# Optimization experiments

Hardware: AMD Instinct MI355X
Metric: run time of the kernel (lower is better)

The kernel has to match this reference:

```python
import jax, jax.numpy as jnp
import numpy as np

NEG_SLOPE = 0.01  # nn.LeakyReLU default

N = 100000
E = 1600000
D_IN = 128
D_OUT = 128


def setup_inputs() -> dict:
    key = jax.random.key(0)
    ks = jax.random.split(key, 8)
    features = jax.random.normal(ks[0], (N, D_IN), dtype=jnp.float32)
    adj_rows = jax.random.randint(ks[1], (E,), 0, N, dtype=jnp.int64)
    adj_cols = jax.random.randint(ks[2], (E,), 0, N, dtype=jnp.int64)
    adj_vals = jax.random.uniform(ks[3], (E,), dtype=jnp.float32)
    s1 = 1.0 / np.sqrt(D_IN)
    W1 = jax.random.uniform(ks[4], (D_IN, D_OUT), jnp.float32, -s1, s1)
    b1 = jax.random.uniform(ks[5], (D_OUT,), jnp.float32, -s1, s1)
    W2 = jax.random.uniform(ks[6], (D_IN, D_OUT), jnp.float32, -s1, s1)
    b2 = jax.random.uniform(ks[7], (D_OUT,), jnp.float32, -s1, s1)
    return {"features": features, "adj_rows": adj_rows, "adj_cols": adj_cols,
            "adj_vals": adj_vals, "W1": W1, "b1": b1, "W2": W2, "b2": b2}


def reference(features, adj_rows, adj_cols, adj_vals, W1, b1, W2, b2):
    # h_neigh = adj @ features  (COO SpMM via gather + segment_sum)
    msgs = adj_vals[:, None] * features[adj_cols]          # [E, D_IN]
    h_neigh = jax.ops.segment_sum(msgs, adj_rows, num_segments=features.shape[0])
    term1 = (features + h_neigh) @ W1 + b1                 # W1(features + h_neigh)
    term2 = (features * h_neigh) @ W2 + b2                 # W2(features * h_neigh)
    pre = term1 + term2
    return jnp.where(pre >= 0, pre, NEG_SLOPE * pre)       # leaky_relu
```

## Files before the change

kernel.cpp:

```cpp
#include <hip/hip_runtime.h>

#define D 128
#define BM 64

typedef short short8 __attribute__((ext_vector_type(8)));
typedef unsigned short ushort8_t __attribute__((ext_vector_type(8)));
typedef float f32x4 __attribute__((ext_vector_type(4)));

__device__ __forceinline__ unsigned short f2bf(float x) {
    unsigned u = __float_as_uint(x);
    unsigned r = (u + 0x7fffu + ((u >> 16) & 1u)) >> 16;
    return (unsigned short)r;
}
__device__ __forceinline__ float bf2f(unsigned short u) {
    return __uint_as_float(((unsigned)u) << 16);
}

__global__ __launch_bounds__(256) void fconv_kernel(
    const float4* __restrict__ feat4, ushort4* __restrict__ fbf4, int total)
{
    int i = blockIdx.x * 256 + threadIdx.x;
    if (i < total) {
        float4 v = feat4[i];
        fbf4[i] = make_ushort4(f2bf(v.x), f2bf(v.y), f2bf(v.z), f2bf(v.w));
    }
}

__global__ __launch_bounds__(256) void wconv_kernel(
    const float* __restrict__ W1, const float* __restrict__ W2,
    unsigned short* __restrict__ WT)
{
    int idx = blockIdx.x * 256 + threadIdx.x;
    int c = idx & 127;
    int k = idx >> 7;
    float w = (k < 128) ? W1[k * 128 + c] : W2[(k - 128) * 128 + c];
    WT[c * 256 + k] = f2bf(w);
}


__global__ __launch_bounds__(256) void bucket_hist_kernel(
    const int* __restrict__ rows, int* __restrict__ bcnt, int E, int nb, int epb)
{
    __shared__ int cnt[1024];
    int t = threadIdx.x;
    for (int i = t; i < nb; i += 256) cnt[i] = 0;
    __syncthreads();
    int e0 = blockIdx.x * epb;
    int e1 = e0 + epb; if (e1 > E) e1 = E;
    for (int e = e0 + t; e < e1; e += 256) atomicAdd(&cnt[rows[e] >> 7], 1);
    __syncthreads();
    for (int i = t; i < nb; i += 256)
        if (cnt[i]) atomicAdd(&bcnt[i], cnt[i]);
}

__global__ __launch_bounds__(1024) void bucket_scan_kernel(
    const int* __restrict__ bcnt, int* __restrict__ bstart,
    int* __restrict__ bcur, int nb, int E)
{
    __shared__ int wsum[16];
    int tid = threadIdx.x, lane = tid & 63, wid = tid >> 6;
    int x = (tid < nb) ? bcnt[tid] : 0;
    int v = x;
    #pragma unroll
    for (int off = 1; off < 64; off <<= 1) {
        int y = __shfl_up(v, off, 64);
        if (lane >= off) v += y;
    }
    if (lane == 63) wsum[wid] = v;
    __syncthreads();
    if (wid == 0 && lane < 16) {
        int s = wsum[lane];
        #pragma unroll
        for (int off = 1; off < 16; off <<= 1) {
            int y = __shfl_up(s, off, 64);
            if (lane >= off) s += y;
        }
        wsum[lane] = s;
    }
    __syncthreads();
    int wexcl = wid ? wsum[wid - 1] : 0;
    int excl = wexcl + v - x;
    if (tid < nb) { bstart[tid] = excl; bcur[tid] = excl; }
    if (tid == 0) bstart[nb] = E;
}

__global__ __launch_bounds__(256) void bucket_scatter_kernel(
    const int* __restrict__ rows, const int* __restrict__ cols,
    const float* __restrict__ vals, int* __restrict__ bcur,
    uint2* __restrict__ bsedge, int E, int nb)
{
    __shared__ int cnt[1024];
    __shared__ int base[1024];
    int t = threadIdx.x;
    int e0 = blockIdx.x * 4096;
    for (int i = t; i < nb; i += 256) cnt[i] = 0;
    __syncthreads();
    #pragma unroll
    for (int q = 0; q < 16; ++q) {
        int e = e0 + t + q * 256;
        if (e < E) atomicAdd(&cnt[rows[e] >> 7], 1);
    }
    __syncthreads();
    for (int i = t; i < nb; i += 256) {
        int c = cnt[i];
        if (c) { base[i] = atomicAdd(&bcur[i], c); cnt[i] = 0; }
    }
    __syncthreads();
    #pragma unroll
    for (int q = 0; q < 16; ++q) {
        int e = e0 + t + q * 256;
        if (e < E) {
            int r = rows[e];
            int b = r >> 7;
            int pos = base[b] + atomicAdd(&cnt[b], 1);
            bsedge[pos] = make_uint2(((unsigned)(r & 127) << 17) | (unsigned)cols[e],
                                     __float_as_uint(vals[e]));
        }
    }
}

__global__ __launch_bounds__(256) void bucket_sort_kernel(
    const uint2* __restrict__ bsedge,
    const int* __restrict__ bstart,
    uint2* __restrict__ sedge,
    int* __restrict__ row_start,
    int N, int E)
{
    __shared__ int cnt[128];
    __shared__ int base[128];
    const int b = blockIdx.x;
    const int t = threadIdx.x;
    const int s = bstart[b], e = bstart[b + 1];
    if (t < 128) cnt[t] = 0;
    __syncthreads();
    for (int j = s + t; j < e; j += 256)
        atomicAdd(&cnt[bsedge[j].x >> 17], 1);
    __syncthreads();
    if (t < 64) {
        int c0 = cnt[2 * t], c1 = cnt[2 * t + 1];
        int pair = c0 + c1;
        int v = pair;
        #pragma unroll
        for (int off = 1; off < 64; off <<= 1) {
            int y = __shfl_up(v, off, 64);
            if (t >= off) v += y;
        }
        int excl = v - pair;
        base[2 * t]     = excl;
        base[2 * t + 1] = excl + c0;
        cnt[2 * t] = 0;
        cnt[2 * t + 1] = 0;
    }
    __syncthreads();
    const int r0 = b << 7;
    if (t < 128 && r0 + t < N) row_start[r0 + t] = s + base[t];
    if (b == 0 && t == 0) row_start[N] = E;
    for (int j = s + t; j < e; j += 256) {
        uint2 ed = bsedge[j];
        int rl = ed.x >> 17;
        int p = atomicAdd(&cnt[rl], 1);
        sedge[s + base[rl] + p] = make_uint2(ed.x & 0x1FFFFu, ed.y);
    }
}

__global__ __launch_bounds__(256) void spmm_gemm16_kernel(
    const float4* __restrict__ feat4,
    const ushort8_t* __restrict__ fbf8,
    const int* __restrict__ row_start,
    const uint2* __restrict__ sedge,
    const unsigned short* __restrict__ WT,
    const float* __restrict__ b1, const float* __restrict__ b2,
    float* __restrict__ out, int N)
{
    __shared__ __align__(16) unsigned char am_raw[16 * 512];

    const int tid = threadIdx.x;
    const int block0 = blockIdx.x * 16;
    const int rq = tid >> 4;
    const int l  = tid & 15;

    int row = block0 + rq;
    float acc[8] = {};
    float f[8] = {};
    if (row < N) {
        int s = row_start[row];
        int e = row_start[row + 1];
        int j = s;
        for (; j + 3 < e; j += 4) {
            uint2 e0 = sedge[j],     e1 = sedge[j + 1];
            uint2 e2 = sedge[j + 2], e3 = sedge[j + 3];
            ushort8_t f0 = fbf8[(size_t)e0.x * 16 + l];
            ushort8_t f1 = fbf8[(size_t)e1.x * 16 + l];
            ushort8_t f2 = fbf8[(size_t)e2.x * 16 + l];
            ushort8_t f3 = fbf8[(size_t)e3.x * 16 + l];
            float v0 = __uint_as_float(e0.y), v1 = __uint_as_float(e1.y);
            float v2 = __uint_as_float(e2.y), v3 = __uint_as_float(e3.y);
            #pragma unroll
            for (int q = 0; q < 8; ++q) {
                acc[q] = fmaf(v0, bf2f(f0[q]), acc[q]);
                acc[q] = fmaf(v1, bf2f(f1[q]), acc[q]);
                acc[q] = fmaf(v2, bf2f(f2[q]), acc[q]);
                acc[q] = fmaf(v3, bf2f(f3[q]), acc[q]);
            }
        }
        for (; j < e; ++j) {
            uint2 e0 = sedge[j];
            float v = __uint_as_float(e0.y);
            ushort8_t f0 = fbf8[(size_t)e0.x * 16 + l];
            #pragma unroll
            for (int q = 0; q < 8; ++q) acc[q] = fmaf(v, bf2f(f0[q]), acc[q]);
        }
        float4 fa = feat4[(size_t)row * 32 + 2 * l];
        float4 fb = feat4[(size_t)row * 32 + 2 * l + 1];
        f[0] = fa.x; f[1] = fa.y; f[2] = fa.z; f[3] = fa.w;
        f[4] = fb.x; f[5] = fb.y; f[6] = fb.z; f[7] = fb.w;
    }
    ushort8_t av, mv;
    #pragma unroll
    for (int q = 0; q < 8; ++q) {
        av[q] = f2bf(f[q] + acc[q]);
        mv[q] = f2bf(f[q] * acc[q]);
    }
    {
        int swz = (rq & 7) << 4;
        unsigned char* rowp = am_raw + rq * 512;
        *(ushort8_t*)(rowp + ((16 * l) ^ swz))       = av;
        *(ushort8_t*)(rowp + 256 + ((16 * l) ^ swz)) = mv;
    }
    __syncthreads();

    const int lane = tid & 63;
    const int w    = tid >> 6;
    const int l15  = lane & 15;
    const int lk   = lane >> 4;
    const int rswz = (l15 & 7) << 4;

    f32x4 gacc[2] = {};
    const char* WTc = (const char*)WT;
    const unsigned char* arow = am_raw + l15 * 512;

    #pragma unroll
    for (int ks = 0; ks < 8; ++ks) {
        int kbyte = ks * 64 + lk * 16;
        short8 a = *(const short8*)(arow + (kbyte ^ rswz));
        #pragma unroll
        for (int nc = 0; nc < 2; ++nc) {
            int col = w * 32 + nc * 16 + l15;
            short8 b = *(const short8*)(WTc + col * 512 + kbyte);
            gacc[nc] = __builtin_amdgcn_mfma_f32_16x16x32_bf16(a, b, gacc[nc], 0, 0, 0);
        }
    }

    #pragma unroll
    for (int nc = 0; nc < 2; ++nc) {
        int col = w * 32 + nc * 16 + l15;
        float bias = b1[col] + b2[col];
        int rbase = block0 + lk * 4;
        #pragma unroll
        for (int r = 0; r < 4; ++r) {
            int orow = rbase + r;
            if (orow < N) {
                float v = gacc[nc][r] + bias;
                out[orow * 128 + col] = (v >= 0.f) ? v : 0.01f * v;
            }
        }
    }
}

__global__ __launch_bounds__(256) void spmm_ab_kernel(
    const float4* __restrict__ feat4,
    const ushort8_t* __restrict__ fbf8,
    const int* __restrict__ row_start,
    const uint2* __restrict__ sedge,
    unsigned char* __restrict__ ambf, int N)
{
    int t = blockIdx.x * 256 + threadIdx.x;
    int row = t >> 4;
    int l   = t & 15;
    if (row >= N) return;

    int s = row_start[row];
    int e = row_start[row + 1];

    float acc[8] = {};
    int j = s;
    for (; j + 1 < e; j += 2) {
        uint2 e0 = sedge[j], e1 = sedge[j + 1];
        float v0 = __uint_as_float(e0.y), v1 = __uint_as_float(e1.y);
        ushort8_t f0 = fbf8[(size_t)e0.x * 16 + l];
        ushort8_t f1 = fbf8[(size_t)e1.x * 16 + l];
        #pragma unroll
        for (int q = 0; q < 8; ++q) {
            acc[q] = fmaf(v0, bf2f(f0[q]), acc[q]);
            acc[q] = fmaf(v1, bf2f(f1[q]), acc[q]);
        }
    }
    if (j < e) {
        uint2 e0 = sedge[j];
        float v = __uint_as_float(e0.y);
        ushort8_t f = fbf8[(size_t)e0.x * 16 + l];
        #pragma unroll
        for (int q = 0; q < 8; ++q) acc[q] = fmaf(v, bf2f(f[q]), acc[q]);
    }

    float4 fa = feat4[(size_t)row * 32 + 2 * l];
    float4 fb = feat4[(size_t)row * 32 + 2 * l + 1];
    float f[8] = { fa.x, fa.y, fa.z, fa.w, fb.x, fb.y, fb.z, fb.w };

    ushort8_t av, mv;
    #pragma unroll
    for (int q = 0; q < 8; ++q) {
        av[q] = f2bf(f[q] + acc[q]);
        mv[q] = f2bf(f[q] * acc[q]);
    }

    int swz = (row & 7) << 4;
    unsigned char* rowp = ambf + (size_t)row * 512;
    *(ushort8_t*)(rowp + ((16 * l) ^ swz))       = av;
    *(ushort8_t*)(rowp + 256 + ((16 * l) ^ swz)) = mv;
}

__global__ __launch_bounds__(256) void mfma_gemm2_kernel(
    const unsigned char* __restrict__ ambf,
    const unsigned short* __restrict__ WT,
    const float* __restrict__ b1, const float* __restrict__ b2,
    float* __restrict__ out, int N)
{
    __shared__ __align__(16) unsigned char am_raw[64 * 512];

    const int tid = threadIdx.x;
    const int block0 = blockIdx.x * BM;

    const short8* src = (const short8*)(ambf + (size_t)block0 * 512);
    short8* dst = (short8*)am_raw;
    #pragma unroll
    for (int it = 0; it < 8; ++it) {
        int idx = tid + it * 256;
        dst[idx] = src[idx];
    }
    __syncthreads();

    const int lane = tid & 63;
    const int w    = tid >> 6;
    const int wr   = w >> 1;
    const int wc   = w & 1;
    const int l15  = lane & 15;
    const int lk   = lane >> 4;
    const int rswz = (l15 & 7) << 4;

    f32x4 acc[2][4] = {};

    const char* WTc = (const char*)WT;
    const unsigned char* arow0 = am_raw + (wr * 32 + l15) * 512;
    const unsigned char* arow1 = arow0 + 16 * 512;

    #pragma unroll
    for (int ks = 0; ks < 8; ++ks) {
        int kbyte = ks * 64 + lk * 16;
        int akoff = kbyte ^ rswz;
        short8 a0 = *(const short8*)(arow0 + akoff);
        short8 a1 = *(const short8*)(arow1 + akoff);
        short8 bfr[4];
        #pragma unroll
        for (int nc = 0; nc < 4; ++nc) {
            int col = wc * 64 + nc * 16 + l15;
            bfr[nc] = *(const short8*)(WTc + col * 512 + kbyte);
        }
        #pragma unroll
        for (int nc = 0; nc < 4; ++nc) {
            acc[0][nc] = __builtin_amdgcn_mfma_f32_16x16x32_bf16(a0, bfr[nc], acc[0][nc], 0, 0, 0);
            acc[1][nc] = __builtin_amdgcn_mfma_f32_16x16x32_bf16(a1, bfr[nc], acc[1][nc], 0, 0, 0);
        }
    }

    #pragma unroll
    for (int nc = 0; nc < 4; ++nc) {
        int col = wc * 64 + nc * 16 + l15;
        float bias = b1[col] + b2[col];
        #pragma unroll
        for (int mr = 0; mr < 2; ++mr) {
            int rbase = block0 + wr * 32 + mr * 16 + lk * 4;
            #pragma unroll
            for (int r = 0; r < 4; ++r) {
                int row = rbase + r;
                if (row < N) {
                    float v = acc[mr][nc][r] + bias;
                    out[row * 128 + col] = (v >= 0.f) ? v : 0.01f * v;
                }
            }
        }
    }
}

__global__ __launch_bounds__(256) void hist_kernel(
    const int* __restrict__ rows, int* __restrict__ counts, int E)
{
    int e = blockIdx.x * 256 + threadIdx.x;
    if (e < E) atomicAdd(&counts[rows[e]], 1);
}

__global__ __launch_bounds__(256) void scan_pass1(
    const int* __restrict__ counts, int* __restrict__ btot, int N)
{
    int tid = threadIdx.x;
    int i = blockIdx.x * 1024 + tid * 4;
    int s = 0;
    if (i + 3 < N) {
        int4 v = *(const int4*)(counts + i);
        s = v.x + v.y + v.z + v.w;
    } else {
        for (int q = 0; q < 4; ++q) if (i + q < N) s += counts[i + q];
    }
    #pragma unroll
    for (int off = 32; off >= 1; off >>= 1) s += __shfl_down(s, off, 64);
    __shared__ int ws[4];
    if ((tid & 63) == 0) ws[tid >> 6] = s;
    __syncthreads();
    if (tid == 0) btot[blockIdx.x] = ws[0] + ws[1] + ws[2] + ws[3];
}

__global__ __launch_bounds__(1024) void scan_pass2(
    const int* __restrict__ btot, int* __restrict__ boff, int nb)
{
    __shared__ int wsum[16];
    int tid = threadIdx.x, lane = tid & 63, wid = tid >> 6;
    int x = (tid < nb) ? btot[tid] : 0;
    int v = x;
    #pragma unroll
    for (int off = 1; off < 64; off <<= 1) {
        int y = __shfl_up(v, off, 64);
        if (lane >= off) v += y;
    }
    if (lane == 63) wsum[wid] = v;
    __syncthreads();
    if (wid == 0 && lane < 16) {
        int s = wsum[lane];
        #pragma unroll
        for (int off = 1; off < 16; off <<= 1) {
            int y = __shfl_up(s, off, 64);
            if (lane >= off) s += y;
        }
        wsum[lane] = s;
    }
    __syncthreads();
    int wexcl = wid ? wsum[wid - 1] : 0;
    if (tid < nb) boff[tid] = wexcl + v - x;
}

__global__ __launch_bounds__(256) void scan_pass3(
    int* __restrict__ row_start, int* __restrict__ cursor,
    const int* __restrict__ boff, int N, int E)
{
    int tid = threadIdx.x;
    int base = blockIdx.x * 1024 + tid * 4;
    int c0 = 0, c1 = 0, c2 = 0, c3 = 0;
    if (base + 3 < N) {
        int4 v = *(const int4*)(row_start + base);
        c0 = v.x; c1 = v.y; c2 = v.z; c3 = v.w;
    } else {
        if (base + 0 < N) c0 = row_start[base + 0];
        if (base + 1 < N) c1 = row_start[base + 1];
        if (base + 2 < N) c2 = row_start[base + 2];
        if (base + 3 < N) c3 = row_start[base + 3];
    }
    int s0 = c0, s1 = s0 + c1, s2 = s1 + c2, s3 = s2 + c3;
    int lane = tid & 63, wid = tid >> 6;
    int v = s3;
    #pragma unroll
    for (int off = 1; off < 64; off <<= 1) {
        int y = __shfl_up(v, off, 64);
        if (lane >= off) v += y;
    }
    __shared__ int ws[4];
    if (lane == 63) ws[wid] = v;
    __syncthreads();
    int wexcl = 0;
    for (int q = 0; q < wid; ++q) wexcl += ws[q];
    int texcl = wexcl + (v - s3) + boff[blockIdx.x];
    int e0 = texcl, e1 = texcl + s0, e2 = texcl + s1, e3 = texcl + s2;
    if (base + 0 < N) { row_start[base + 0] = e0; cursor[base + 0] = e0; }
    if (base + 1 < N) { row_start[base + 1] = e1; cursor[base + 1] = e1; }
    if (base + 2 < N) { row_start[base + 2] = e2; cursor[base + 2] = e2; }
    if (base + 3 < N) { row_start[base + 3] = e3; cursor[base + 3] = e3; }
    if (blockIdx.x == 0 && tid == 0) row_start[N] = E;
}

__global__ __launch_bounds__(256) void scatter_sort_kernel(
    const int* __restrict__ rows, const int* __restrict__ cols,
    const float* __restrict__ vals, int* __restrict__ cursor,
    uint2* __restrict__ sedge, int E)
{
    int e = blockIdx.x * 256 + threadIdx.x;
    if (e < E) {
        int r = rows[e];
        int p = atomicAdd(&cursor[r], 1);
        sedge[p] = make_uint2((unsigned)cols[e], __float_as_uint(vals[e]));
    }
}

__global__ __launch_bounds__(256) void spmm_kernel(
    const float2* __restrict__ feat2,
    const int* __restrict__ row_start,
    const uint2* __restrict__ sedge,
    float2* __restrict__ h2, int N)
{
    int gw = (blockIdx.x * 256 + threadIdx.x) >> 6;
    int lane = threadIdx.x & 63;
    if (gw >= N) return;
    int s = row_start[gw];
    int e = row_start[gw + 1];
    float2 acc = make_float2(0.f, 0.f);
    int j = s;
    for (; j + 1 < e; j += 2) {
        uint2 e0 = sedge[j], e1 = sedge[j + 1];
        float v0 = __uint_as_float(e0.y), v1 = __uint_as_float(e1.y);
        float2 f0 = feat2[(size_t)e0.x * 64 + lane];
        float2 f1 = feat2[(size_t)e1.x * 64 + lane];
        acc.x = fmaf(v0, f0.x, acc.x);
        acc.y = fmaf(v0, f0.y, acc.y);
        acc.x = fmaf(v1, f1.x, acc.x);
        acc.y = fmaf(v1, f1.y, acc.y);
    }
    if (j < e) {
        uint2 e0 = sedge[j];
        float v = __uint_as_float(e0.y);
        float2 f = feat2[(size_t)e0.x * 64 + lane];
        acc.x = fmaf(v, f.x, acc.x);
        acc.y = fmaf(v, f.y, acc.y);
    }
    h2[(size_t)gw * 64 + lane] = acc;
}

__global__ __launch_bounds__(256) void mfma_gemm_kernel(
    const float4* __restrict__ feat4, const float4* __restrict__ h4,
    const unsigned short* __restrict__ WT,
    const float* __restrict__ b1, const float* __restrict__ b2,
    float* __restrict__ out, int N)
{
    __shared__ __align__(16) unsigned char am_raw[64 * 512];
    const int tid = threadIdx.x;
    const int block0 = blockIdx.x * BM;
    #pragma unroll
    for (int it = 0; it < 8; ++it) {
        int idx  = tid + it * 256;
        int node = idx >> 5;
        int p    = idx & 31;
        int g    = block0 + node;
        float4 fv = make_float4(0.f, 0.f, 0.f, 0.f);
        float4 hv = make_float4(0.f, 0.f, 0.f, 0.f);
        if (g < N) { fv = feat4[g * 32 + p]; hv = h4[g * 32 + p]; }
        ushort4 av = make_ushort4(f2bf(fv.x + hv.x), f2bf(fv.y + hv.y),
                                  f2bf(fv.z + hv.z), f2bf(fv.w + hv.w));
        ushort4 mv = make_ushort4(f2bf(fv.x * hv.x), f2bf(fv.y * hv.y),
                                  f2bf(fv.z * hv.z), f2bf(fv.w * hv.w));
        int swz = (node & 7) << 4;
        *(ushort4*)(am_raw + node * 512 + ((p * 8) ^ swz))       = av;
        *(ushort4*)(am_raw + node * 512 + ((256 + p * 8) ^ swz)) = mv;
    }
    __syncthreads();
    const int lane = tid & 63;
    const int w    = tid >> 6;
    const int wr   = w >> 1;
    const int wc   = w & 1;
    const int l15  = lane & 15;
    const int lk   = lane >> 4;
    const int rswz = (l15 & 7) << 4;
    f32x4 acc[2][4] = {};
    const char* WTc = (const char*)WT;
    const unsigned char* arow0 = am_raw + (wr * 32 + l15) * 512;
    const unsigned char* arow1 = arow0 + 16 * 512;
    #pragma unroll
    for (int ks = 0; ks < 8; ++ks) {
        int kbyte = ks * 64 + lk * 16;
        int akoff = kbyte ^ rswz;
        short8 a0 = *(const short8*)(arow0 + akoff);
        short8 a1 = *(const short8*)(arow1 + akoff);
        short8 bfr[4];
        #pragma unroll
        for (int nc = 0; nc < 4; ++nc) {
            int col = wc * 64 + nc * 16 + l15;
            bfr[nc] = *(const short8*)(WTc + col * 512 + kbyte);
        }
        #pragma unroll
        for (int nc = 0; nc < 4; ++nc) {
            acc[0][nc] = __builtin_amdgcn_mfma_f32_16x16x32_bf16(a0, bfr[nc], acc[0][nc], 0, 0, 0);
            acc[1][nc] = __builtin_amdgcn_mfma_f32_16x16x32_bf16(a1, bfr[nc], acc[1][nc], 0, 0, 0);
        }
    }
    #pragma unroll
    for (int nc = 0; nc < 4; ++nc) {
        int col = wc * 64 + nc * 16 + l15;
        float bias = b1[col] + b2[col];
        #pragma unroll
        for (int mr = 0; mr < 2; ++mr) {
            int rbase = block0 + wr * 32 + mr * 16 + lk * 4;
            #pragma unroll
            for (int r = 0; r < 4; ++r) {
                int row = rbase + r;
                if (row < N) {
                    float v = acc[mr][nc][r] + bias;
                    out[row * 128 + col] = (v >= 0.f) ? v : 0.01f * v;
                }
            }
        }
    }
}

__global__ __launch_bounds__(256) void edge_scatter_kernel(
    const float4* __restrict__ feat4, const int* __restrict__ rows,
    const int* __restrict__ cols, const float* __restrict__ vals,
    float* __restrict__ h, int E)
{
    int idx = blockIdx.x * 256 + threadIdx.x;
    if (idx >= E * 32) return;
    int e = idx >> 5;
    int p = idx & 31;
    int r = rows[e];
    int c = cols[e];
    float v = vals[e];
    float4 f = feat4[c * 32 + p];
    float* hr = h + (long long)r * D + p * 4;
    unsafeAtomicAdd(hr + 0, v * f.x);
    unsafeAtomicAdd(hr + 1, v * f.y);
    unsafeAtomicAdd(hr + 2, v * f.z);
    unsafeAtomicAdd(hr + 3, v * f.w);
}

__global__ __launch_bounds__(256) void fused_gemm_kernel(
    const float* __restrict__ feat, const float* __restrict__ h,
    const float* __restrict__ W1, const float* __restrict__ b1,
    const float* __restrict__ W2, const float* __restrict__ b2,
    float* __restrict__ out, int N)
{
    __shared__ float a_lds[BM][D];
    __shared__ float m_lds[BM][D];
    const int tid = threadIdx.x;
    const int block0 = blockIdx.x * BM;
    const float4* feat4 = (const float4*)feat;
    const float4* h4    = (const float4*)h;
    #pragma unroll
    for (int it = 0; it < 8; ++it) {
        int idx  = tid + it * 256;
        int node = idx >> 5;
        int p    = idx & 31;
        int gnode = block0 + node;
        float4 fv = make_float4(0.f, 0.f, 0.f, 0.f);
        float4 hv = make_float4(0.f, 0.f, 0.f, 0.f);
        if (gnode < N) { fv = feat4[gnode * 32 + p]; hv = h4[gnode * 32 + p]; }
        float4 av = make_float4(fv.x + hv.x, fv.y + hv.y, fv.z + hv.z, fv.w + hv.w);
        float4 mv = make_float4(fv.x * hv.x, fv.y * hv.y, fv.z * hv.z, fv.w * hv.w);
        *(float4*)&a_lds[node][p * 4] = av;
        *(float4*)&m_lds[node][p * 4] = mv;
    }
    __syncthreads();
    const int c = tid & 31;
    const int g = tid >> 5;
    float acc[8][4] = {};
    const float4* W1v = (const float4*)W1;
    const float4* W2v = (const float4*)W2;
    for (int k = 0; k < D; ++k) {
        float4 w1 = W1v[k * 32 + c];
        float4 w2 = W2v[k * 32 + c];
        #pragma unroll
        for (int t = 0; t < 8; ++t) {
            float av = a_lds[g + 8 * t][k];
            float mv = m_lds[g + 8 * t][k];
            acc[t][0] = fmaf(av, w1.x, fmaf(mv, w2.x, acc[t][0]));
            acc[t][1] = fmaf(av, w1.y, fmaf(mv, w2.y, acc[t][1]));
            acc[t][2] = fmaf(av, w1.z, fmaf(mv, w2.z, acc[t][2]));
            acc[t][3] = fmaf(av, w1.w, fmaf(mv, w2.w, acc[t][3]));
        }
    }
    float4 bb1 = ((const float4*)b1)[c];
    float4 bb2 = ((const float4*)b2)[c];
    const float bx = bb1.x + bb2.x, by = bb1.y + bb2.y;
    const float bz = bb1.z + bb2.z, bw = bb1.w + bb2.w;
    #pragma unroll
    for (int t = 0; t < 8; ++t) {
        int gnode = block0 + g + 8 * t;
        if (gnode >= N) continue;
        float4 o;
        o.x = acc[t][0] + bx; o.y = acc[t][1] + by;
        o.z = acc[t][2] + bz; o.w = acc[t][3] + bw;
        o.x = (o.x >= 0.f) ? o.x : 0.01f * o.x;
        o.y = (o.y >= 0.f) ? o.y : 0.01f * o.y;
        o.z = (o.z >= 0.f) ? o.z : 0.01f * o.z;
        o.w = (o.w >= 0.f) ? o.w : 0.01f * o.w;
        ((float4*)out)[gnode * 32 + c] = o;
    }
}

extern "C" void kernel_launch(void* const* d_in, const int* in_sizes, int n_in,
                              void* d_out, int out_size, void* d_ws, size_t ws_size,
                              hipStream_t stream) {
    const float* feat = (const float*)d_in[0];
    const int*   rows = (const int*)d_in[1];
    const int*   cols = (const int*)d_in[2];
    const float* vals = (const float*)d_in[3];
    const float* W1   = (const float*)d_in[4];
    const float* b1   = (const float*)d_in[5];
    const float* W2   = (const float*)d_in[6];
    const float* b2   = (const float*)d_in[7];

    const int N = in_sizes[0] / D;
    const int E = in_sizes[1];
    float* out = (float*)d_out;

    const int NBK  = (N + 127) >> 7;
    const int Npad = NBK << 7;

    size_t off = 0;
    unsigned short* featbf = (unsigned short*)d_ws;                off += (size_t)N * D * 2;
    off = (off + 15) & ~(size_t)15;
    uint2* sedge = (uint2*)((char*)d_ws + off);                    off += (size_t)E * 8;
    unsigned short* WT = (unsigned short*)((char*)d_ws + off);     off += 128 * 256 * 2;
    int* row_start = (int*)((char*)d_ws + off);                    off += (size_t)(N + 1) * 4;
    off = (off + 15) & ~(size_t)15;
    uint2* bsedge = (uint2*)((char*)d_ws + off);                   off += (size_t)E * 8;
    int* bcnt   = (int*)((char*)d_ws + off);                       off += (size_t)NBK * 4;
    int* bstart = (int*)((char*)d_ws + off);                       off += (size_t)(NBK + 1) * 4;
    int* bcur   = (int*)((char*)d_ws + off);                       off += (size_t)NBK * 4;
    size_t need1a = off;

    if (ws_size >= need1a && NBK <= 1024 && N <= (1 << 17)) {
        hipMemsetAsync(bcnt, 0, (size_t)NBK * sizeof(int), stream);
        fconv_kernel<<<(N * 32 + 255) / 256, 256, 0, stream>>>(
            (const float4*)feat, (ushort4*)featbf, N * 32);
        wconv_kernel<<<128, 256, 0, stream>>>(W1, W2, WT);
        int epb = (E + 255) / 256;
        bucket_hist_kernel<<<256, 256, 0, stream>>>(rows, bcnt, E, NBK, epb);
        bucket_scan_kernel<<<1, 1024, 0, stream>>>(bcnt, bstart, bcur, NBK, E);
        bucket_scatter_kernel<<<(E + 4095) / 4096, 256, 0, stream>>>(
            rows, cols, vals, bcur, bsedge, E, NBK);
        bucket_sort_kernel<<<NBK, 256, 0, stream>>>(
            bsedge, bstart, sedge, row_start, N, E);
        spmm_gemm16_kernel<<<(N + 15) / 16, 256, 0, stream>>>(
            (const float4*)feat, (const ushort8_t*)featbf, row_start, sedge,
            WT, b1, b2, out, N);
        return;
    }

    const int NB = (N + 1023) / 1024;
    off = 0;
    unsigned char* ambf = (unsigned char*)d_ws;                    off += (size_t)Npad * 512;
    featbf = (unsigned short*)((char*)d_ws + off);                 off += (size_t)N * D * 2;
    off = (off + 15) & ~(size_t)15;
    sedge = (uint2*)((char*)d_ws + off);                           off += (size_t)E * 8;
    WT = (unsigned short*)((char*)d_ws + off);                     off += 128 * 256 * 2;
    row_start = (int*)((char*)d_ws + off);                         off += (size_t)(N + 1) * 4;
    off = (off + 15) & ~(size_t)15;
    int* cursor = (int*)((char*)d_ws + off);                       off += (size_t)N * 4;
    int* btot = (int*)((char*)d_ws + off);                         off += (size_t)NB * 4;
    int* boff = (int*)((char*)d_ws + off);                         off += (size_t)NB * 4;
    size_t need1b = off;

    if (ws_size >= need1b && NB <= 1024) {
        hipMemsetAsync(row_start, 0, (size_t)(N + 1) * sizeof(int), stream);
        fconv_kernel<<<(N * 32 + 255) / 256, 256, 0, stream>>>(
            (const float4*)feat, (ushort4*)featbf, N * 32);
        wconv_kernel<<<128, 256, 0, stream>>>(W1, W2, WT);
        hist_kernel<<<(E + 255) / 256, 256, 0, stream>>>(rows, row_start, E);
        scan_pass1<<<NB, 256, 0, stream>>>(row_start, btot, N);
        scan_pass2<<<1, 1024, 0, stream>>>(btot, boff, NB);
        scan_pass3<<<NB, 256, 0, stream>>>(row_start, cursor, boff, N, E);
        scatter_sort_kernel<<<(E + 255) / 256, 256, 0, stream>>>(
            rows, cols, vals, cursor, sedge, E);
        spmm_ab_kernel<<<(N * 16 + 255) / 256, 256, 0, stream>>>(
            (const float4*)feat, (const ushort8_t*)featbf, row_start, sedge,
            ambf, N);
        mfma_gemm2_kernel<<<(N + BM - 1) / BM, 256, 0, stream>>>(
            ambf, WT, b1, b2, out, N);
        return;
    }

    off = 0;
    float* h = (float*)d_ws;                           off += (size_t)N * D * 4;
    int* row_start2 = (int*)((char*)d_ws + off);       off += (size_t)(N + 1) * 4;
    int* cursor2    = (int*)((char*)d_ws + off);       off += (size_t)N * 4;
    off = (off + 15) & ~(size_t)15;
    uint2* sedge2   = (uint2*)((char*)d_ws + off);     off += (size_t)E * 8;
    off = (off + 15) & ~(size_t)15;
    unsigned short* WT2 = (unsigned short*)((char*)d_ws + off); off += 128 * 256 * 2;
    int* btot2 = (int*)((char*)d_ws + off);            off += (size_t)NB * 4;
    int* boff2 = (int*)((char*)d_ws + off);            off += (size_t)NB * 4;
    size_t need2 = off;

    if (ws_size >= need2 && NB <= 1024) {
        hipMemsetAsync(row_start2, 0, (size_t)(N + 1) * sizeof(int), stream);
        wconv_kernel<<<128, 256, 0, stream>>>(W1, W2, WT2);
        hist_kernel<<<(E + 255) / 256, 256, 0, stream>>>(rows, row_start2, E);
        scan_pass1<<<NB, 256, 0, stream>>>(row_start2, btot2, N);
        scan_pass2<<<1, 1024, 0, stream>>>(btot2, boff2, NB);
        scan_pass3<<<NB, 256, 0, stream>>>(row_start2, cursor2, boff2, N, E);
        scatter_sort_kernel<<<(E + 255) / 256, 256, 0, stream>>>(
            rows, cols, vals, cursor2, sedge2, E);
        spmm_kernel<<<(N * 64 + 255) / 256, 256, 0, stream>>>(
            (const float2*)feat, row_start2, sedge2, (float2*)h, N);
        mfma_gemm_kernel<<<(N + BM - 1) / BM, 256, 0, stream>>>(
            (const float4*)feat, (const float4*)h, WT2, b1, b2, out, N);
        return;
    }

    size_t hbytes = (size_t)N * D * sizeof(float);
    float* hh = (ws_size >= hbytes) ? (float*)d_ws : out;
    hipMemsetAsync(hh, 0, hbytes, stream);
    edge_scatter_kernel<<<((size_t)E * 32 + 255) / 256, 256, 0, stream>>>(
        (const float4*)feat, rows, cols, vals, hh, E);
    fused_gemm_kernel<<<(N + BM - 1) / BM, 256, 0, stream>>>(
        feat, hh, W1, b1, W2, b2, out, N);
}
```

Baseline: 184.6 us.

## Fuse preprocessing kernels, unroll gather by 8, read own features in bf16

Merges the feature bf16 conversion, weight transpose/convert, and row-bucket histogram into one prep kernel, saving two launches and letting the independent work overlap. The SpMM gather loop gains an 8-wide unrolled path that issues more independent loads before accumulating, to hide gather latency. The row's own features are now read from the bf16 copy instead of fp32, which halves that read but adds rounding error to the features+h and features*h terms.

```diff
diff --git a/kernel.cpp b/kernel.cpp
--- a/kernel.cpp
+++ b/kernel.cpp
@@ -14,6 +14,41 @@
 }
 __device__ __forceinline__ float bf2f(unsigned short u) {
     return __uint_as_float(((unsigned)u) << 16);
+}
+
+__global__ __launch_bounds__(256) void prep_kernel(
+    const float4* __restrict__ feat4, ushort4* __restrict__ fbf4, int nf4,
+    const float* __restrict__ W1, const float* __restrict__ W2,
+    unsigned short* __restrict__ WT,
+    const int* __restrict__ rows, int* __restrict__ bcnt,
+    int E, int nb, int epb)
+{
+    __shared__ int cnt[1024];
+    const int t = threadIdx.x;
+    const int b = blockIdx.x;
+    for (int i = t; i < nb; i += 256) cnt[i] = 0;
+    __syncthreads();
+
+    int e0 = b * epb;
+    int e1 = e0 + epb; if (e1 > E) e1 = E;
+    for (int e = e0 + t; e < e1; e += 256) atomicAdd(&cnt[rows[e] >> 7], 1);
+
+    for (int i = b * 256 + t; i < nf4; i += 256 * 256) {
+        float4 v = feat4[i];
+        fbf4[i] = make_ushort4(f2bf(v.x), f2bf(v.y), f2bf(v.z), f2bf(v.w));
+    }
+
+    if (b < 128) {
+        int idx = b * 256 + t;
+        int c = idx & 127;
+        int k = idx >> 7;
+        float w = (k < 128) ? W1[k * 128 + c] : W2[(k - 128) * 128 + c];
+        WT[c * 256 + k] = f2bf(w);
+    }
+
+    __syncthreads();
+    for (int i = t; i < nb; i += 256)
+        if (cnt[i]) atomicAdd(&bcnt[i], cnt[i]);
 }
 
 __global__ __launch_bounds__(256) void fconv_kernel(
@@ -35,22 +70,6 @@
     int k = idx >> 7;
     float w = (k < 128) ? W1[k * 128 + c] : W2[(k - 128) * 128 + c];
     WT[c * 256 + k] = f2bf(w);
-}
-
-
-__global__ __launch_bounds__(256) void bucket_hist_kernel(
-    const int* __restrict__ rows, int* __restrict__ bcnt, int E, int nb, int epb)
-{
-    __shared__ int cnt[1024];
-    int t = threadIdx.x;
-    for (int i = t; i < nb; i += 256) cnt[i] = 0;
-    __syncthreads();
-    int e0 = blockIdx.x * epb;
-    int e1 = e0 + epb; if (e1 > E) e1 = E;
-    for (int e = e0 + t; e < e1; e += 256) atomicAdd(&cnt[rows[e] >> 7], 1);
-    __syncthreads();
-    for (int i = t; i < nb; i += 256)
-        if (cnt[i]) atomicAdd(&bcnt[i], cnt[i]);
 }
 
 __global__ __launch_bounds__(1024) void bucket_scan_kernel(
@@ -164,7 +183,6 @@
 }
 
 __global__ __launch_bounds__(256) void spmm_gemm16_kernel(
-    const float4* __restrict__ feat4,
     const ushort8_t* __restrict__ fbf8,
     const int* __restrict__ row_start,
     const uint2* __restrict__ sedge,
@@ -186,6 +204,22 @@
         int s = row_start[row];
         int e = row_start[row + 1];
         int j = s;
+        for (; j + 7 < e; j += 8) {
+            uint2 ed[8];
+            #pragma unroll
+            for (int q = 0; q < 8; ++q) ed[q] = sedge[j + q];
+            ushort8_t ff[8];
+            #pragma unroll
+            for (int q = 0; q < 8; ++q)
+                ff[q] = fbf8[(size_t)ed[q].x * 16 + l];
+            #pragma unroll
+            for (int q = 0; q < 8; ++q) {
+                float v = __uint_as_float(ed[q].y);
+                #pragma unroll
+                for (int p = 0; p < 8; ++p)
+                    acc[p] = fmaf(v, bf2f(ff[q][p]), acc[p]);
+            }
+        }
         for (; j + 3 < e; j += 4) {
             uint2 e0 = sedge[j],     e1 = sedge[j + 1];
             uint2 e2 = sedge[j + 2], e3 = sedge[j + 3];
@@ -196,11 +230,11 @@
             float v0 = __uint_as_float(e0.y), v1 = __uint_as_float(e1.y);
             float v2 = __uint_as_float(e2.y), v3 = __uint_as_float(e3.y);
             #pragma unroll
-            for (int q = 0; q < 8; ++q) {
-                acc[q] = fmaf(v0, bf2f(f0[q]), acc[q]);
-                acc[q] = fmaf(v1, bf2f(f1[q]), acc[q]);
-                acc[q] = fmaf(v2, bf2f(f2[q]), acc[q]);
-                acc[q] = fmaf(v3, bf2f(f3[q]), acc[q]);
+            for (int p = 0; p < 8; ++p) {
+                acc[p] = fmaf(v0, bf2f(f0[p]), acc[p]);
+                acc[p] = fmaf(v1, bf2f(f1[p]), acc[p]);
+                acc[p] = fmaf(v2, bf2f(f2[p]), acc[p]);
+                acc[p] = fmaf(v3, bf2f(f3[p]), acc[p]);
             }
         }
         for (; j < e; ++j) {
@@ -208,12 +242,11 @@
             float v = __uint_as_float(e0.y);
             ushort8_t f0 = fbf8[(size_t)e0.x * 16 + l];
             #pragma unroll
-            for (int q = 0; q < 8; ++q) acc[q] = fmaf(v, bf2f(f0[q]), acc[q]);
-        }
-        float4 fa = feat4[(size_t)row * 32 + 2 * l];
-        float4 fb = feat4[(size_t)row * 32 + 2 * l + 1];
-        f[0] = fa.x; f[1] = fa.y; f[2] = fa.z; f[3] = fa.w;
-        f[4] = fb.x; f[5] = fb.y; f[6] = fb.z; f[7] = fb.w;
+            for (int p = 0; p < 8; ++p) acc[p] = fmaf(v, bf2f(f0[p]), acc[p]);
+        }
+        ushort8_t fown = fbf8[(size_t)row * 16 + l];
+        #pragma unroll
+        for (int p = 0; p < 8; ++p) f[p] = bf2f(fown[p]);
     }
     ushort8_t av, mv;
     #pragma unroll
@@ -724,18 +757,17 @@
 
     if (ws_size >= need1a && NBK <= 1024 && N <= (1 << 17)) {
         hipMemsetAsync(bcnt, 0, (size_t)NBK * sizeof(int), stream);
-        fconv_kernel<<<(N * 32 + 255) / 256, 256, 0, stream>>>(
-            (const float4*)feat, (ushort4*)featbf, N * 32);
-        wconv_kernel<<<128, 256, 0, stream>>>(W1, W2, WT);
         int epb = (E + 255) / 256;
-        bucket_hist_kernel<<<256, 256, 0, stream>>>(rows, bcnt, E, NBK, epb);
+        prep_kernel<<<256, 256, 0, stream>>>(
+            (const float4*)feat, (ushort4*)featbf, N * 32,
+            W1, W2, WT, rows, bcnt, E, NBK, epb);
         bucket_scan_kernel<<<1, 1024, 0, stream>>>(bcnt, bstart, bcur, NBK, E);
         bucket_scatter_kernel<<<(E + 4095) / 4096, 256, 0, stream>>>(
             rows, cols, vals, bcur, bsedge, E, NBK);
         bucket_sort_kernel<<<NBK, 256, 0, stream>>>(
             bsedge, bstart, sedge, row_start, N, E);
         spmm_gemm16_kernel<<<(N + 15) / 16, 256, 0, stream>>>(
-            (const float4*)feat, (const ushort8_t*)featbf, row_start, sedge,
+            (const ushort8_t*)featbf, row_start, sedge,
             WT, b1, b2, out, N);
         return;
     }
```

Result: no change. 182.9 us (-0.9%).
